# Kernel tuning notes

Hardware: AMD Instinct MI355X
Metric: run time of the kernel (lower is better)

The kernel has to match this reference:

```python
import math
import jax, jax.numpy as jnp
import numpy as np

B, T, C, FD, K, V = 8, 2048, 256, 256, 128, 256

def setup_inputs() -> dict:
    key = jax.random.key(0)
    ks = jax.random.split(key, 8)
    s = 0.02
    return {
        "inp": jax.random.normal(ks[0], (B, T, C), jnp.float32),
        "feature": jax.random.normal(ks[1], (B, T, FD), jnp.float32),
        "Wq": jax.random.normal(ks[2], (C + FD, K), jnp.float32) * s,
        "bq": jnp.zeros((K,), jnp.float32),
        "Wk": jax.random.normal(ks[3], (C, K), jnp.float32) * s,
        "bk": jnp.zeros((K,), jnp.float32),
        "Wv": jax.random.normal(ks[4], (C, V), jnp.float32) * s,
        "bv": jnp.zeros((V,), jnp.float32),
    }

def reference(inp, feature, Wq, bq, Wk, bk, Wv, bv):
    # inp: [B,T,C], feature: [B,T,FD]
    t = inp.shape[1]
    q = jnp.concatenate([inp, feature], axis=-1) @ Wq + bq   # [B,T,K]
    k = inp @ Wk + bk                                        # [B,T,K]
    v = inp @ Wv + bv                                        # [B,T,V]
    # scores[b, j, i] = q_j . k_i ; original masks where i > j (strict upper tri)
    scores = jnp.einsum('bjk,bik->bji', q, k)                # [B,T,T]
    mask = jnp.triu(jnp.ones((t, t), dtype=bool), k=1)       # mask[j,i] = i > j
    scores = jnp.where(mask[None], -jnp.inf, scores) / math.sqrt(K)
    # NOTE: original softmax is over dim=1 (the query/row axis), not the key axis
    attn = jax.nn.softmax(scores, axis=1)                    # [B,T,T]
    out = jnp.einsum('bji,biv->bjv', attn, v)                # [B,T,V]
    return jnp.concatenate([inp, out], axis=-1)              # [B,T,C+V]
```

## Files before the change

### kernel.cpp

```cpp
#include <hip/hip_runtime.h>
#include <hip/hip_bf16.h>
#include <cstdint>

#define Bb  8
#define Tt  2048
#define Cc  256
#define FDd 256
#define Kk  128
#define Vv  256
#define BT  (Bb * Tt)
#define NTRI 136

#define INV_SQRT_K 0.08838834764831845f

typedef __bf16 bf16x8 __attribute__((ext_vector_type(8)));
typedef __bf16 bf16x4 __attribute__((ext_vector_type(4)));
typedef float  f32x4  __attribute__((ext_vector_type(4)));

__device__ __forceinline__ void gload16(const void* g, void* l) {
  __builtin_amdgcn_global_load_lds(
      (const __attribute__((address_space(1))) void*)g,
      (__attribute__((address_space(3))) void*)l, 16, 0, 0);
}

__global__ __launch_bounds__(256) void prepw_kernel(
    const float4* __restrict__ inp4, const float4* __restrict__ feat4,
    float4* __restrict__ out4, bf16x4* __restrict__ inpB4,
    bf16x4* __restrict__ featB4,
    const float* __restrict__ Wq, const float* __restrict__ Wk,
    const float* __restrict__ Wv, __bf16* __restrict__ Wqt,
    __bf16* __restrict__ Wkt, __bf16* __restrict__ Wvt)
{
  if (blockIdx.x < 4096) {
    const int g = blockIdx.x * 256 + threadIdx.x;
    const int row = g >> 6, c = g & 63;
    const float4 x = inp4[g];
    out4[(size_t)row * 128 + c] = x;
    bf16x4 xb; xb[0] = (__bf16)x.x; xb[1] = (__bf16)x.y; xb[2] = (__bf16)x.z; xb[3] = (__bf16)x.w;
    inpB4[g] = xb;
    const float4 f = feat4[g];
    bf16x4 fb; fb[0] = (__bf16)f.x; fb[1] = (__bf16)f.y; fb[2] = (__bf16)f.z; fb[3] = (__bf16)f.w;
    featB4[g] = fb;
  } else {
    const int g = (blockIdx.x - 4096) * 256 + threadIdx.x;
    if (g < 65536) {
      const int n = g >> 9, k = g & 511;
      Wqt[g] = (__bf16)Wq[k * 128 + n];
    } else if (g < 98304) {
      const int h = g - 65536;
      const int n = h >> 8, k = h & 255;
      Wkt[h] = (__bf16)Wk[k * 128 + n];
    } else {
      const int h = g - 98304;
      const int n = h >> 8, k = h & 255;
      Wvt[h] = (__bf16)Wv[k * 256 + n];
    }
  }
}

__global__ __launch_bounds__(256, 3) void qkv_mfma_kernel(
    const __bf16* __restrict__ inpB, const __bf16* __restrict__ featB,
    const __bf16* __restrict__ Wqt, const __bf16* __restrict__ Wkt,
    const __bf16* __restrict__ Wvt,
    const float* __restrict__ bq, const float* __restrict__ bk,
    const float* __restrict__ bv,
    __bf16* __restrict__ qb, __bf16* __restrict__ kb, __bf16* __restrict__ vT)
{
  __shared__ __bf16 Atile[128 * 64];
  __shared__ __bf16 Btile[128 * 64];
  const int panel = blockIdx.y;
  const int m0 = blockIdx.x * 128;
  const int lane = threadIdx.x & 63, wave = threadIdx.x >> 6;
  const int cl = lane & 15, quad = lane >> 4;
  const int jl0 = (wave >> 1) * 64;
  const int vl0 = (wave & 1) * 64;

  const __bf16* Wt; const float* bias; int kblocks;
  if (panel == 0)      { Wt = Wqt; bias = bq; kblocks = 8; }
  else if (panel == 1) { Wt = Wkt; bias = bk; kblocks = 4; }
  else                 { Wt = Wvt + (size_t)(panel - 2) * 128 * 256;
                         bias = bv + (panel - 2) * 128; kblocks = 4; }
  const int Kd = kblocks * 64;

  const int lrow = lane >> 3;
  const int lchunk = ((lane & 7) ^ lrow) * 8;

  f32x4 acc[4][4];
#pragma unroll
  for (int mt = 0; mt < 4; ++mt)
#pragma unroll
    for (int nt = 0; nt < 4; ++nt) acc[mt][nt] = (f32x4){0.f, 0.f, 0.f, 0.f};

  for (int kb = 0; kb < kblocks; ++kb) {
    const __bf16* Asrc = (panel == 0 && kb >= 4) ? featB : inpB;
    const int koff = (panel == 0 && kb >= 4) ? (kb - 4) * 64 : kb * 64;
    __syncthreads();
#pragma unroll
    for (int t = 0; t < 4; ++t) {
      const int r0 = wave * 32 + t * 8;
      gload16(Asrc + (size_t)(m0 + r0 + lrow) * 256 + koff + lchunk, Atile + r0 * 64);
      gload16(Wt + (size_t)(r0 + lrow) * Kd + kb * 64 + lchunk, Btile + r0 * 64);
    }
    __syncthreads();
#pragma unroll
    for (int ks = 0; ks < 2; ++ks) {
      bf16x8 af[4], bfr[4];
#pragma unroll
      for (int mt = 0; mt < 4; ++mt) {
        const int jlr = jl0 + mt * 16 + cl;
        af[mt] = *(const bf16x8*)(Atile + jlr * 64 + (((ks * 4 + quad) ^ (jlr & 7)) * 8));
      }
#pragma unroll
      for (int nt = 0; nt < 4; ++nt) {
        const int vlr = vl0 + nt * 16 + cl;
        bfr[nt] = *(const bf16x8*)(Btile + vlr * 64 + (((ks * 4 + quad) ^ (vlr & 7)) * 8));
      }
#pragma unroll
      for (int mt = 0; mt < 4; ++mt)
#pragma unroll
        for (int nt = 0; nt < 4; ++nt)
          acc[mt][nt] = __builtin_amdgcn_mfma_f32_16x16x32_bf16(af[mt], bfr[nt], acc[mt][nt], 0, 0, 0);
    }
  }

  if (panel < 2) {
    __bf16* dst = (panel == 0) ? qb : kb;
    const float scale = (panel == 0) ? INV_SQRT_K : 1.0f;
#pragma unroll
    for (int mt = 0; mt < 4; ++mt) {
      const int row = m0 + jl0 + mt * 16 + quad * 4;
#pragma unroll
      for (int nt = 0; nt < 4; ++nt) {
        const int col = vl0 + nt * 16 + cl;
        const float bs = bias[col];
#pragma unroll
        for (int r = 0; r < 4; ++r)
          dst[(size_t)(row + r) * Kk + col] = (__bf16)((acc[mt][nt][r] + bs) * scale);
      }
    }
  } else {
    const int b = m0 >> 11;
#pragma unroll
    for (int mt = 0; mt < 4; ++mt) {
      const int t0 = (m0 & (Tt - 1)) + jl0 + mt * 16 + quad * 4;
#pragma unroll
      for (int nt = 0; nt < 4; ++nt) {
        const int vcol = (panel - 2) * 128 + vl0 + nt * 16 + cl;
        const float bs = bias[vl0 + nt * 16 + cl];
        bf16x4 v4;
#pragma unroll
        for (int r = 0; r < 4; ++r) v4[r] = (__bf16)(acc[mt][nt][r] + bs);
        *(bf16x4*)(vT + (size_t)(b * Vv + vcol) * Tt + t0) = v4;
      }
    }
  }
}

__global__ __launch_bounds__(256, 2) void sexp_kernel(
    const __bf16* __restrict__ qb, const __bf16* __restrict__ kb,
    __bf16* __restrict__ expS, float* __restrict__ partialD)
{
  __shared__ __bf16 tiles[2 * 128 * 128];
  __shared__ float lcs[4][64];
  __bf16* Qtile = tiles;
  __bf16* Ktile = tiles + 128 * 128;
  float*  P     = (float*)tiles;

  const int b = blockIdx.x, l = blockIdx.y;
  int jt = 0, base = 0;
  while (base + jt + 1 <= l) { base += jt + 1; ++jt; }
  const int it = l - base;

  const int lane = threadIdx.x & 63, wave = threadIdx.x >> 6;
  const int cl = lane & 15, quad = lane >> 4;
  const int jl0 = (wave >> 1) * 64;
  const int il0 = (wave & 1) * 64;
  const size_t rowbase = (size_t)b * Tt;

  {
    const int srow = lane >> 4;
    const int cslot = lane & 15;
    const __bf16* qsrc = qb + (rowbase + jt * 128) * Kk;
    const __bf16* ksrc = kb + (rowbase + it * 128) * Kk;
#pragma unroll
    for (int t = 0; t < 8; ++t) {
      const int r0 = wave * 32 + t * 4;
      const int row = r0 + srow;
      const int cg = (cslot ^ (row & 7)) * 8;
      gload16(qsrc + (size_t)row * Kk + cg, Qtile + r0 * 128);
      gload16(ksrc + (size_t)row * Kk + cg, Ktile + r0 * 128);
    }
  }
  __syncthreads();

  f32x4 acc[4][4];
#pragma unroll
  for (int mt = 0; mt < 4; ++mt)
#pragma unroll
    for (int nt = 0; nt < 4; ++nt) acc[mt][nt] = (f32x4){0.f, 0.f, 0.f, 0.f};

#pragma unroll
  for (int s = 0; s < 4; ++s) {
    bf16x8 af[4], bfr[4];
#pragma unroll
    for (int mt = 0; mt < 4; ++mt) {
      const int jlr = jl0 + mt * 16 + cl;
      af[mt] = *(const bf16x8*)(Qtile + jlr * 128 + (((s * 4 + quad) ^ (jlr & 7)) * 8));
    }
#pragma unroll
    for (int nt = 0; nt < 4; ++nt) {
      const int ilr = il0 + nt * 16 + cl;
      bfr[nt] = *(const bf16x8*)(Ktile + ilr * 128 + (((s * 4 + quad) ^ (ilr & 7)) * 8));
    }
#pragma unroll
    for (int mt = 0; mt < 4; ++mt)
#pragma unroll
      for (int nt = 0; nt < 4; ++nt)
        acc[mt][nt] = __builtin_amdgcn_mfma_f32_16x16x32_bf16(af[mt], bfr[nt], acc[mt][nt], 0, 0, 0);
  }
  __syncthreads();

  const bool diag = (it == jt);
  float cs[4] = {0.f, 0.f, 0.f, 0.f};
#pragma unroll
  for (int mt = 0; mt < 4; ++mt) {
    const int jl = jl0 + mt * 16 + quad * 4;
#pragma unroll
    for (int nt = 0; nt < 4; ++nt) {
      const int il = il0 + nt * 16 + cl;
#pragma unroll
      for (int r = 0; r < 4; ++r) {
        float p = __expf(acc[mt][nt][r]);
        if (diag && il > (jl + r)) p = 0.f;
        cs[nt] += (float)(__bf16)p;
        P[(jl + r) * 128 + il] = p;
      }
    }
  }
#pragma unroll
  for (int nt = 0; nt < 4; ++nt) {
    cs[nt] += __shfl_xor(cs[nt], 16);
    cs[nt] += __shfl_xor(cs[nt], 32);
  }
  if (quad == 0) {
#pragma unroll
    for (int nt = 0; nt < 4; ++nt) lcs[wave][nt * 16 + cl] = cs[nt];
  }
  __syncthreads();

  __bf16* slot = expS + ((size_t)(b * NTRI + l)) * (128 * 128);
  {
    const int srow = lane >> 4;
    const int c0 = (lane & 15) * 8;
#pragma unroll
    for (int t = 0; t < 8; ++t) {
      const int row = wave * 32 + t * 4 + srow;
      const f32x4 p0 = *(const f32x4*)(P + row * 128 + c0);
      const f32x4 p1 = *(const f32x4*)(P + row * 128 + c0 + 4);
      bf16x8 pb;
#pragma unroll
      for (int u = 0; u < 4; ++u) { pb[u] = (__bf16)p0[u]; pb[4 + u] = (__bf16)p1[u]; }
      *(bf16x8*)(slot + (size_t)row * 128 + c0) = pb;
    }
  }

  const int tid = threadIdx.x;
  if (tid < 128) {
    const int w0 = (tid < 64) ? 0 : 1;
    const int lc = tid & 63;
    const float s = lcs[w0][lc] + lcs[w0 + 2][lc];
    partialD[((size_t)b * 16 + jt) * Tt + it * 128 + tid] = s;
  }
}

__global__ __launch_bounds__(256) void dvscale_kernel(
    const float* __restrict__ partialD, bf16x8* __restrict__ vT8)
{
  __shared__ float rec[32];
  const int b = blockIdx.x, ic = blockIdx.y;
  const int i0 = ic * 32;
  const int tid = threadIdx.x;
  if (tid < 32) {
    const int i = i0 + tid;
    float s = 0.f;
#pragma unroll
    for (int jt = 0; jt < 16; ++jt) s += partialD[((size_t)b * 16 + jt) * Tt + i];
    rec[tid] = 1.0f / s;
  }
  __syncthreads();
  const int iu = tid & 3, v0 = tid >> 2;
#pragma unroll
  for (int p = 0; p < 4; ++p) {
    const int v = v0 + p * 64;
    const size_t idx = ((size_t)b * Vv + v) * (Tt / 8) + (i0 >> 3) + iu;
    bf16x8 x = vT8[idx];
    const int rb = iu * 8;
#pragma unroll
    for (int t = 0; t < 8; ++t) x[t] = (__bf16)((float)x[t] * rec[rb + t]);
    vT8[idx] = x;
  }
}

__global__ __launch_bounds__(256, 4) void pvgemm_kernel(
    const __bf16* __restrict__ expS, const __bf16* __restrict__ vT,
    float* __restrict__ out)
{
  __shared__ __bf16 At[2][128 * 64];
  __shared__ __bf16 Bt[2][64 * 64];
  const int b = blockIdx.x;
  const int p = blockIdx.y >> 2;
  const int nq = blockIdx.y & 3;
  const int lane = threadIdx.x & 63, wave = threadIdx.x >> 6;
  const int cl = lane & 15, quad = lane >> 4;
  const int jl0 = (wave >> 1) * 64;
  const int vl0 = (wave & 1) * 32;
  const int lrow = lane >> 3;
  const int lchunk = ((lane & 7) ^ lrow) * 8;
  const __bf16* vbase = vT + ((size_t)b * Vv + nq * 64) * Tt;

#pragma unroll
  for (int sp = 0; sp < 2; ++sp) {
    const int jt = sp ? p : 15 - p;
    const int kblocks = (jt + 1) * 2;
    const size_t slotbase = (size_t)(b * NTRI + (jt * (jt + 1)) / 2) * 16384;

    f32x4 acc[4][2];
#pragma unroll
    for (int mt = 0; mt < 4; ++mt)
#pragma unroll
      for (int nt = 0; nt < 2; ++nt) acc[mt][nt] = (f32x4){0.f, 0.f, 0.f, 0.f};

    {
      const __bf16* Ag = expS + slotbase;
#pragma unroll
      for (int t = 0; t < 4; ++t) {
        const int r0 = wave * 32 + t * 8;
        gload16(Ag + (size_t)(r0 + lrow) * 128 + lchunk, At[0] + r0 * 64);
      }
#pragma unroll
      for (int t = 0; t < 2; ++t) {
        const int r0 = wave * 16 + t * 8;
        gload16(vbase + (size_t)(r0 + lrow) * Tt + lchunk, Bt[0] + r0 * 64);
      }
    }
    __syncthreads();

    int buf = 0;
    for (int kb = 0; kb < kblocks; ++kb) {
      if (kb + 1 < kblocks) {
        const int kn = kb + 1;
        const __bf16* Ag = expS + slotbase + (size_t)(kn >> 1) * 16384 + (kn & 1) * 64;
        const int i0 = kn * 64;
#pragma unroll
        for (int t = 0; t < 4; ++t) {
          const int r0 = wave * 32 + t * 8;
          gload16(Ag + (size_t)(r0 + lrow) * 128 + lchunk, At[buf ^ 1] + r0 * 64);
        }
#pragma unroll
        for (int t = 0; t < 2; ++t) {
          const int r0 = wave * 16 + t * 8;
          gload16(vbase + (size_t)(r0 + lrow) * Tt + i0 + lchunk, Bt[buf ^ 1] + r0 * 64);
        }
      }
#pragma unroll
      for (int ks = 0; ks < 2; ++ks) {
        bf16x8 af[4], bfr[2];
#pragma unroll
        for (int mt = 0; mt < 4; ++mt) {
          const int jlr = jl0 + mt * 16 + cl;
          af[mt] = *(const bf16x8*)(At[buf] + jlr * 64 + (((ks * 4 + quad) ^ (jlr & 7)) * 8));
        }
#pragma unroll
        for (int nt = 0; nt < 2; ++nt) {
          const int vlr = vl0 + nt * 16 + cl;
          bfr[nt] = *(const bf16x8*)(Bt[buf] + vlr * 64 + (((ks * 4 + quad) ^ (vlr & 7)) * 8));
        }
#pragma unroll
        for (int mt = 0; mt < 4; ++mt)
#pragma unroll
          for (int nt = 0; nt < 2; ++nt)
            acc[mt][nt] = __builtin_amdgcn_mfma_f32_16x16x32_bf16(af[mt], bfr[nt], acc[mt][nt], 0, 0, 0);
      }
      __syncthreads();
      buf ^= 1;
    }

    float* orow = out + ((size_t)b * Tt + jt * 128 + jl0) * (size_t)(Cc + Vv)
                + Cc + nq * 64 + vl0;
#pragma unroll
    for (int mt = 0; mt < 4; ++mt)
#pragma unroll
      for (int nt = 0; nt < 2; ++nt)
#pragma unroll
        for (int r = 0; r < 4; ++r)
          orow[(size_t)(mt * 16 + quad * 4 + r) * (Cc + Vv) + nt * 16 + cl] = acc[mt][nt][r];
  }
}

extern "C" void kernel_launch(void* const* d_in, const int* in_sizes, int n_in,
                              void* d_out, int out_size, void* d_ws, size_t ws_size,
                              hipStream_t stream) {
  const float* inp  = (const float*)d_in[0];
  const float* feat = (const float*)d_in[1];
  const float* Wq   = (const float*)d_in[2];
  const float* bq   = (const float*)d_in[3];
  const float* Wk   = (const float*)d_in[4];
  const float* bk   = (const float*)d_in[5];
  const float* Wv   = (const float*)d_in[6];
  const float* bv   = (const float*)d_in[7];
  float* out = (float*)d_out;

  char* ws = (char*)d_ws;
  __bf16* inpB   = (__bf16*)(ws);
  __bf16* featB  = (__bf16*)(ws + (8u << 20));
  __bf16* qb     = (__bf16*)(ws + (16u << 20));
  __bf16* kb     = (__bf16*)(ws + (20u << 20));
  __bf16* vT     = (__bf16*)(ws + (24u << 20));
  __bf16* Wqt    = (__bf16*)(ws + (32u << 20));
  __bf16* Wkt    = (__bf16*)(ws + (32u << 20) + (128u << 10));
  __bf16* Wvt    = (__bf16*)(ws + (32u << 20) + (192u << 10));
  float*  partialD = (float*)(ws + (33u << 20));
  __bf16* expS     = (__bf16*)(ws + (36u << 20));

  prepw_kernel<<<dim3(4096 + 640), 256, 0, stream>>>(
      (const float4*)inp, (const float4*)feat, (float4*)out,
      (bf16x4*)inpB, (bf16x4*)featB, Wq, Wk, Wv, Wqt, Wkt, Wvt);
  qkv_mfma_kernel<<<dim3(BT / 128, 4), 256, 0, stream>>>(
      inpB, featB, Wqt, Wkt, Wvt, bq, bk, bv, qb, kb, vT);
  sexp_kernel<<<dim3(Bb, NTRI), 256, 0, stream>>>(qb, kb, expS, partialD);
  dvscale_kernel<<<dim3(Bb, 64), 256, 0, stream>>>(partialD, (bf16x8*)vT);
  pvgemm_kernel<<<dim3(Bb, 32), 256, 0, stream>>>(expS, vT, out);
}
```

Measured before the change: 160.1 us.

## Fold softmax reciprocal scaling into PV GEMM and swizzle P staging buffer

Replaces the separate kernel that rescaled the whole bf16 V^T tensor in place with a small reduction kernel that only writes per-key reciprocals; the PV GEMM now multiplies its B fragments by those reciprocals after loading them from LDS. This removes a read-modify-write pass over V but adds float conversions and multiplies, plus global reciprocal loads, inside the GEMM inner loop. It also XOR-swizzles the column index of the fp32 P staging tile in the score kernel to cut LDS bank conflicts between the scattered MFMA-layout writes and the row-vector reads.

```diff
diff --git a/kernel.cpp b/kernel.cpp
--- a/kernel.cpp
+++ b/kernel.cpp
@@ -233,7 +233,8 @@
         float p = __expf(acc[mt][nt][r]);
         if (diag && il > (jl + r)) p = 0.f;
         cs[nt] += (float)(__bf16)p;
-        P[(jl + r) * 128 + il] = p;
+        const int row = jl + r;
+        P[row * 128 + (il ^ (((row >> 2) & 1) << 4))] = p;
       }
     }
   }
@@ -255,8 +256,9 @@
 #pragma unroll
     for (int t = 0; t < 8; ++t) {
       const int row = wave * 32 + t * 4 + srow;
-      const f32x4 p0 = *(const f32x4*)(P + row * 128 + c0);
-      const f32x4 p1 = *(const f32x4*)(P + row * 128 + c0 + 4);
+      const int c0p = c0 ^ (((row >> 2) & 1) << 4);
+      const f32x4 p0 = *(const f32x4*)(P + row * 128 + c0p);
+      const f32x4 p1 = *(const f32x4*)(P + row * 128 + c0p + 4);
       bf16x8 pb;
 #pragma unroll
       for (int u = 0; u < 4; ++u) { pb[u] = (__bf16)p0[u]; pb[4 + u] = (__bf16)p1[u]; }
@@ -273,37 +275,20 @@
   }
 }
 
-__global__ __launch_bounds__(256) void dvscale_kernel(
-    const float* __restrict__ partialD, bf16x8* __restrict__ vT8)
+__global__ __launch_bounds__(256) void dreduce_kernel(
+    const float* __restrict__ partialD, float* __restrict__ recipD)
 {
-  __shared__ float rec[32];
-  const int b = blockIdx.x, ic = blockIdx.y;
-  const int i0 = ic * 32;
-  const int tid = threadIdx.x;
-  if (tid < 32) {
-    const int i = i0 + tid;
-    float s = 0.f;
-#pragma unroll
-    for (int jt = 0; jt < 16; ++jt) s += partialD[((size_t)b * 16 + jt) * Tt + i];
-    rec[tid] = 1.0f / s;
-  }
-  __syncthreads();
-  const int iu = tid & 3, v0 = tid >> 2;
-#pragma unroll
-  for (int p = 0; p < 4; ++p) {
-    const int v = v0 + p * 64;
-    const size_t idx = ((size_t)b * Vv + v) * (Tt / 8) + (i0 >> 3) + iu;
-    bf16x8 x = vT8[idx];
-    const int rb = iu * 8;
-#pragma unroll
-    for (int t = 0; t < 8; ++t) x[t] = (__bf16)((float)x[t] * rec[rb + t]);
-    vT8[idx] = x;
-  }
+  const int g = blockIdx.x * 256 + threadIdx.x;
+  const int b = g >> 11, i = g & (Tt - 1);
+  float s = 0.f;
+#pragma unroll
+  for (int jt = 0; jt < 16; ++jt) s += partialD[((size_t)b * 16 + jt) * Tt + i];
+  recipD[g] = 1.0f / s;
 }
 
 __global__ __launch_bounds__(256, 4) void pvgemm_kernel(
     const __bf16* __restrict__ expS, const __bf16* __restrict__ vT,
-    float* __restrict__ out)
+    const float* __restrict__ recipD, float* __restrict__ out)
 {
   __shared__ __bf16 At[2][128 * 64];
   __shared__ __bf16 Bt[2][64 * 64];
@@ -317,6 +302,7 @@
   const int lrow = lane >> 3;
   const int lchunk = ((lane & 7) ^ lrow) * 8;
   const __bf16* vbase = vT + ((size_t)b * Vv + nq * 64) * Tt;
+  const float* rbase = recipD + (size_t)b * Tt;
 
 #pragma unroll
   for (int sp = 0; sp < 2; ++sp) {
@@ -350,7 +336,7 @@
       if (kb + 1 < kblocks) {
         const int kn = kb + 1;
         const __bf16* Ag = expS + slotbase + (size_t)(kn >> 1) * 16384 + (kn & 1) * 64;
-        const int i0 = kn * 64;
+        const int i0n = kn * 64;
 #pragma unroll
         for (int t = 0; t < 4; ++t) {
           const int r0 = wave * 32 + t * 8;
@@ -359,11 +345,14 @@
 #pragma unroll
         for (int t = 0; t < 2; ++t) {
           const int r0 = wave * 16 + t * 8;
-          gload16(vbase + (size_t)(r0 + lrow) * Tt + i0 + lchunk, Bt[buf ^ 1] + r0 * 64);
+          gload16(vbase + (size_t)(r0 + lrow) * Tt + i0n + lchunk, Bt[buf ^ 1] + r0 * 64);
         }
       }
+      const float* rstep = rbase + kb * 64;
 #pragma unroll
       for (int ks = 0; ks < 2; ++ks) {
+        const f32x4 ra = *(const f32x4*)(rstep + (ks * 4 + quad) * 8);
+        const f32x4 rb = *(const f32x4*)(rstep + (ks * 4 + quad) * 8 + 4);
         bf16x8 af[4], bfr[2];
 #pragma unroll
         for (int mt = 0; mt < 4; ++mt) {
@@ -374,6 +363,11 @@
         for (int nt = 0; nt < 2; ++nt) {
           const int vlr = vl0 + nt * 16 + cl;
           bfr[nt] = *(const bf16x8*)(Bt[buf] + vlr * 64 + (((ks * 4 + quad) ^ (vlr & 7)) * 8));
+#pragma unroll
+          for (int u = 0; u < 4; ++u) {
+            bfr[nt][u]     = (__bf16)((float)bfr[nt][u]     * ra[u]);
+            bfr[nt][4 + u] = (__bf16)((float)bfr[nt][4 + u] * rb[u]);
+          }
         }
 #pragma unroll
         for (int mt = 0; mt < 4; ++mt)
@@ -420,6 +414,7 @@
   __bf16* Wkt    = (__bf16*)(ws + (32u << 20) + (128u << 10));
   __bf16* Wvt    = (__bf16*)(ws + (32u << 20) + (192u << 10));
   float*  partialD = (float*)(ws + (33u << 20));
+  float*  recipD   = (float*)(ws + (35u << 20));
   __bf16* expS     = (__bf16*)(ws + (36u << 20));
 
   prepw_kernel<<<dim3(4096 + 640), 256, 0, stream>>>(
@@ -428,6 +423,6 @@
   qkv_mfma_kernel<<<dim3(BT / 128, 4), 256, 0, stream>>>(
       inpB, featB, Wqt, Wkt, Wvt, bq, bk, bv, qb, kb, vT);
   sexp_kernel<<<dim3(Bb, NTRI), 256, 0, stream>>>(qb, kb, expS, partialD);
-  dvscale_kernel<<<dim3(Bb, 64), 256, 0, stream>>>(partialD, (bf16x8*)vT);
-  pvgemm_kernel<<<dim3(Bb, 32), 256, 0, stream>>>(expS, vT, out);
-}
+  dreduce_kernel<<<dim3(BT / 256), 256, 0, stream>>>(partialD, recipD);
+  pvgemm_kernel<<<dim3(Bb, 32), 256, 0, stream>>>(expS, vT, recipD, out);
+}
```

Measured after the change: 168.1 us. 1.05x slower.

## Split-K the PV GEMM with atomic accumulation and swizzle P staging in LDS

Applied to the files above, without the earlier changes.

The PV GEMM grid is changed from paired row tiles to per-tile chunks of up to eight k-blocks, giving many more blocks with even work. Partial results are combined with relaxed atomic float adds, so the output's V half is zero-initialised in the prep kernel. Separately, the fp32 P staging buffer in the score kernel is XOR-swizzled to reduce LDS bank conflicts. Atomics add traffic and make the summation order nondeterministic.

```diff
diff --git a/kernel.cpp b/kernel.cpp
--- a/kernel.cpp
+++ b/kernel.cpp
@@ -36,6 +36,7 @@
     const int row = g >> 6, c = g & 63;
     const float4 x = inp4[g];
     out4[(size_t)row * 128 + c] = x;
+    out4[(size_t)row * 128 + 64 + c] = (float4){0.f, 0.f, 0.f, 0.f};
     bf16x4 xb; xb[0] = (__bf16)x.x; xb[1] = (__bf16)x.y; xb[2] = (__bf16)x.z; xb[3] = (__bf16)x.w;
     inpB4[g] = xb;
     const float4 f = feat4[g];
@@ -233,7 +234,8 @@
         float p = __expf(acc[mt][nt][r]);
         if (diag && il > (jl + r)) p = 0.f;
         cs[nt] += (float)(__bf16)p;
-        P[(jl + r) * 128 + il] = p;
+        const int row = jl + r;
+        P[row * 128 + (il ^ (((row >> 2) & 1) << 4))] = p;
       }
     }
   }
@@ -255,8 +257,9 @@
 #pragma unroll
     for (int t = 0; t < 8; ++t) {
       const int row = wave * 32 + t * 4 + srow;
-      const f32x4 p0 = *(const f32x4*)(P + row * 128 + c0);
-      const f32x4 p1 = *(const f32x4*)(P + row * 128 + c0 + 4);
+      const int c0p = c0 ^ (((row >> 2) & 1) << 4);
+      const f32x4 p0 = *(const f32x4*)(P + row * 128 + c0p);
+      const f32x4 p1 = *(const f32x4*)(P + row * 128 + c0p + 4);
       bf16x8 pb;
 #pragma unroll
       for (int u = 0; u < 4; ++u) { pb[u] = (__bf16)p0[u]; pb[4 + u] = (__bf16)p1[u]; }
@@ -301,15 +304,21 @@
   }
 }
 
-__global__ __launch_bounds__(256, 4) void pvgemm_kernel(
+__global__ __launch_bounds__(256, 3) void pvgemm_kernel(
     const __bf16* __restrict__ expS, const __bf16* __restrict__ vT,
     float* __restrict__ out)
 {
   __shared__ __bf16 At[2][128 * 64];
   __shared__ __bf16 Bt[2][64 * 64];
   const int b = blockIdx.x;
-  const int p = blockIdx.y >> 2;
   const int nq = blockIdx.y & 3;
+  const int z = blockIdx.y >> 2;
+  int jt = 0, zb = 0;
+  while (zb + (jt >> 2) + 1 <= z) { zb += (jt >> 2) + 1; ++jt; }
+  const int c = z - zb;
+  const int kb0 = c * 8;
+  const int kend = min(kb0 + 8, (jt + 1) * 2);
+
   const int lane = threadIdx.x & 63, wave = threadIdx.x >> 6;
   const int cl = lane & 15, quad = lane >> 4;
   const int jl0 = (wave >> 1) * 64;
@@ -317,84 +326,82 @@
   const int lrow = lane >> 3;
   const int lchunk = ((lane & 7) ^ lrow) * 8;
   const __bf16* vbase = vT + ((size_t)b * Vv + nq * 64) * Tt;
-
-#pragma unroll
-  for (int sp = 0; sp < 2; ++sp) {
-    const int jt = sp ? p : 15 - p;
-    const int kblocks = (jt + 1) * 2;
-    const size_t slotbase = (size_t)(b * NTRI + (jt * (jt + 1)) / 2) * 16384;
-
-    f32x4 acc[4][2];
-#pragma unroll
-    for (int mt = 0; mt < 4; ++mt)
-#pragma unroll
-      for (int nt = 0; nt < 2; ++nt) acc[mt][nt] = (f32x4){0.f, 0.f, 0.f, 0.f};
-
-    {
-      const __bf16* Ag = expS + slotbase;
+  const size_t slotbase = (size_t)(b * NTRI + (jt * (jt + 1)) / 2) * 16384;
+
+  f32x4 acc[4][2];
+#pragma unroll
+  for (int mt = 0; mt < 4; ++mt)
+#pragma unroll
+    for (int nt = 0; nt < 2; ++nt) acc[mt][nt] = (f32x4){0.f, 0.f, 0.f, 0.f};
+
+  {
+    const __bf16* Ag = expS + slotbase + (size_t)(kb0 >> 1) * 16384 + (kb0 & 1) * 64;
+    const int i0 = kb0 * 64;
+#pragma unroll
+    for (int t = 0; t < 4; ++t) {
+      const int r0 = wave * 32 + t * 8;
+      gload16(Ag + (size_t)(r0 + lrow) * 128 + lchunk, At[0] + r0 * 64);
+    }
+#pragma unroll
+    for (int t = 0; t < 2; ++t) {
+      const int r0 = wave * 16 + t * 8;
+      gload16(vbase + (size_t)(r0 + lrow) * Tt + i0 + lchunk, Bt[0] + r0 * 64);
+    }
+  }
+  __syncthreads();
+
+  int buf = 0;
+  for (int kb = kb0; kb < kend; ++kb) {
+    if (kb + 1 < kend) {
+      const int kn = kb + 1;
+      const __bf16* Ag = expS + slotbase + (size_t)(kn >> 1) * 16384 + (kn & 1) * 64;
+      const int i0n = kn * 64;
 #pragma unroll
       for (int t = 0; t < 4; ++t) {
         const int r0 = wave * 32 + t * 8;
-        gload16(Ag + (size_t)(r0 + lrow) * 128 + lchunk, At[0] + r0 * 64);
+        gload16(Ag + (size_t)(r0 + lrow) * 128 + lchunk, At[buf ^ 1] + r0 * 64);
       }
 #pragma unroll
       for (int t = 0; t < 2; ++t) {
         const int r0 = wave * 16 + t * 8;
-        gload16(vbase + (size_t)(r0 + lrow) * Tt + lchunk, Bt[0] + r0 * 64);
-      }
+        gload16(vbase + (size_t)(r0 + lrow) * Tt + i0n + lchunk, Bt[buf ^ 1] + r0 * 64);
+      }
+    }
+#pragma unroll
+    for (int ks = 0; ks < 2; ++ks) {
+      bf16x8 af[4], bfr[2];
+#pragma unroll
+      for (int mt = 0; mt < 4; ++mt) {
+        const int jlr = jl0 + mt * 16 + cl;
+        af[mt] = *(const bf16x8*)(At[buf] + jlr * 64 + (((ks * 4 + quad) ^ (jlr & 7)) * 8));
+      }
+#pragma unroll
+      for (int nt = 0; nt < 2; ++nt) {
+        const int vlr = vl0 + nt * 16 + cl;
+        bfr[nt] = *(const bf16x8*)(Bt[buf] + vlr * 64 + (((ks * 4 + quad) ^ (vlr & 7)) * 8));
+      }
+#pragma unroll
+      for (int mt = 0; mt < 4; ++mt)
+#pragma unroll
+        for (int nt = 0; nt < 2; ++nt)
+          acc[mt][nt] = __builtin_amdgcn_mfma_f32_16x16x32_bf16(af[mt], bfr[nt], acc[mt][nt], 0, 0, 0);
     }
     __syncthreads();
-
-    int buf = 0;
-    for (int kb = 0; kb < kblocks; ++kb) {
-      if (kb + 1 < kblocks) {
-        const int kn = kb + 1;
-        const __bf16* Ag = expS + slotbase + (size_t)(kn >> 1) * 16384 + (kn & 1) * 64;
-        const int i0 = kn * 64;
-#pragma unroll
-        for (int t = 0; t < 4; ++t) {
-          const int r0 = wave * 32 + t * 8;
-          gload16(Ag + (size_t)(r0 + lrow) * 128 + lchunk, At[buf ^ 1] + r0 * 64);
-        }
-#pragma unroll
-        for (int t = 0; t < 2; ++t) {
-          const int r0 = wave * 16 + t * 8;
-          gload16(vbase + (size_t)(r0 + lrow) * Tt + i0 + lchunk, Bt[buf ^ 1] + r0 * 64);
-        }
-      }
-#pragma unroll
-      for (int ks = 0; ks < 2; ++ks) {
-        bf16x8 af[4], bfr[2];
-#pragma unroll
-        for (int mt = 0; mt < 4; ++mt) {
-          const int jlr = jl0 + mt * 16 + cl;
-          af[mt] = *(const bf16x8*)(At[buf] + jlr * 64 + (((ks * 4 + quad) ^ (jlr & 7)) * 8));
-        }
-#pragma unroll
-        for (int nt = 0; nt < 2; ++nt) {
-          const int vlr = vl0 + nt * 16 + cl;
-          bfr[nt] = *(const bf16x8*)(Bt[buf] + vlr * 64 + (((ks * 4 + quad) ^ (vlr & 7)) * 8));
-        }
-#pragma unroll
-        for (int mt = 0; mt < 4; ++mt)
-#pragma unroll
-          for (int nt = 0; nt < 2; ++nt)
-            acc[mt][nt] = __builtin_amdgcn_mfma_f32_16x16x32_bf16(af[mt], bfr[nt], acc[mt][nt], 0, 0, 0);
-      }
-      __syncthreads();
-      buf ^= 1;
-    }
-
-    float* orow = out + ((size_t)b * Tt + jt * 128 + jl0) * (size_t)(Cc + Vv)
-                + Cc + nq * 64 + vl0;
-#pragma unroll
-    for (int mt = 0; mt < 4; ++mt)
-#pragma unroll
-      for (int nt = 0; nt < 2; ++nt)
-#pragma unroll
-        for (int r = 0; r < 4; ++r)
-          orow[(size_t)(mt * 16 + quad * 4 + r) * (Cc + Vv) + nt * 16 + cl] = acc[mt][nt][r];
-  }
+    buf ^= 1;
+  }
+
+  float* orow = out + ((size_t)b * Tt + jt * 128 + jl0) * (size_t)(Cc + Vv)
+              + Cc + nq * 64 + vl0;
+#pragma unroll
+  for (int mt = 0; mt < 4; ++mt)
+#pragma unroll
+    for (int nt = 0; nt < 2; ++nt)
+#pragma unroll
+      for (int r = 0; r < 4; ++r) {
+        float* addr = orow + (size_t)(mt * 16 + quad * 4 + r) * (Cc + Vv) + nt * 16 + cl;
+        __hip_atomic_fetch_add(addr, acc[mt][nt][r], __ATOMIC_RELAXED,
+                               __HIP_MEMORY_SCOPE_AGENT);
+      }
 }
 
 extern "C" void kernel_launch(void* const* d_in, const int* in_sizes, int n_in,
@@ -429,5 +436,5 @@
       inpB, featB, Wqt, Wkt, Wvt, bq, bk, bv, qb, kb, vT);
   sexp_kernel<<<dim3(Bb, NTRI), 256, 0, stream>>>(qb, kb, expS, partialD);
   dvscale_kernel<<<dim3(Bb, 64), 256, 0, stream>>>(partialD, (bf16x8*)vT);
-  pvgemm_kernel<<<dim3(Bb, 32), 256, 0, stream>>>(expS, vT, out);
-}
+  pvgemm_kernel<<<dim3(Bb, 160), 256, 0, stream>>>(expS, vT, out);
+}
```

Result: slower. 170.3 us (+6.4%).

## Split PV GEMM into 64-row tiles and swizzle sexp LDS staging

Applied to the files above, without the earlier changes.

The PV GEMM kernel now works on 64-row output tiles instead of 128-row ones. It pairs tile p with tile 31-p so each block does the same total amount of work, and it launches twice as many blocks, with smaller LDS A buffers and fewer accumulators per wave. The aim is better occupancy and load balance on the triangular workload. The sexp kernel also XOR-swizzles the float scratch tile P to reduce LDS bank conflicts on the write and readback. A trailing barrier is added between the two sub-problems, and each expS A tile is now loaded once per 64-row half, so the same bytes may be fetched more often.

```diff
diff --git a/kernel.cpp b/kernel.cpp
--- a/kernel.cpp
+++ b/kernel.cpp
@@ -233,7 +233,8 @@
         float p = __expf(acc[mt][nt][r]);
         if (diag && il > (jl + r)) p = 0.f;
         cs[nt] += (float)(__bf16)p;
-        P[(jl + r) * 128 + il] = p;
+        const int row = jl + r;
+        P[row * 128 + (il ^ (((row >> 2) & 1) << 4))] = p;
       }
     }
   }
@@ -255,8 +256,9 @@
 #pragma unroll
     for (int t = 0; t < 8; ++t) {
       const int row = wave * 32 + t * 4 + srow;
-      const f32x4 p0 = *(const f32x4*)(P + row * 128 + c0);
-      const f32x4 p1 = *(const f32x4*)(P + row * 128 + c0 + 4);
+      const int c0p = c0 ^ (((row >> 2) & 1) << 4);
+      const f32x4 p0 = *(const f32x4*)(P + row * 128 + c0p);
+      const f32x4 p1 = *(const f32x4*)(P + row * 128 + c0p + 4);
       bf16x8 pb;
 #pragma unroll
       for (int u = 0; u < 4; ++u) { pb[u] = (__bf16)p0[u]; pb[4 + u] = (__bf16)p1[u]; }
@@ -305,14 +307,14 @@
     const __bf16* __restrict__ expS, const __bf16* __restrict__ vT,
     float* __restrict__ out)
 {
-  __shared__ __bf16 At[2][128 * 64];
+  __shared__ __bf16 At[2][64 * 64];
   __shared__ __bf16 Bt[2][64 * 64];
   const int b = blockIdx.x;
   const int p = blockIdx.y >> 2;
   const int nq = blockIdx.y & 3;
   const int lane = threadIdx.x & 63, wave = threadIdx.x >> 6;
   const int cl = lane & 15, quad = lane >> 4;
-  const int jl0 = (wave >> 1) * 64;
+  const int jl0 = (wave >> 1) * 32;
   const int vl0 = (wave & 1) * 32;
   const int lrow = lane >> 3;
   const int lchunk = ((lane & 7) ^ lrow) * 8;
@@ -320,53 +322,46 @@
 
 #pragma unroll
   for (int sp = 0; sp < 2; ++sp) {
-    const int jt = sp ? p : 15 - p;
-    const int kblocks = (jt + 1) * 2;
-    const size_t slotbase = (size_t)(b * NTRI + (jt * (jt + 1)) / 2) * 16384;
-
-    f32x4 acc[4][2];
-#pragma unroll
-    for (int mt = 0; mt < 4; ++mt)
+    const int jt64 = sp ? p : 31 - p;
+    const int jt128 = jt64 >> 1;
+    const int rowoff = (jt64 & 1) * 64;
+    const int ksteps = jt64 + 1;
+    const size_t tribase = (size_t)(b * NTRI + (jt128 * (jt128 + 1)) / 2) * 16384;
+
+    f32x4 acc[2][2];
+#pragma unroll
+    for (int mt = 0; mt < 2; ++mt)
 #pragma unroll
       for (int nt = 0; nt < 2; ++nt) acc[mt][nt] = (f32x4){0.f, 0.f, 0.f, 0.f};
 
-    {
-      const __bf16* Ag = expS + slotbase;
-#pragma unroll
-      for (int t = 0; t < 4; ++t) {
-        const int r0 = wave * 32 + t * 8;
-        gload16(Ag + (size_t)(r0 + lrow) * 128 + lchunk, At[0] + r0 * 64);
-      }
-#pragma unroll
-      for (int t = 0; t < 2; ++t) {
-        const int r0 = wave * 16 + t * 8;
-        gload16(vbase + (size_t)(r0 + lrow) * Tt + lchunk, Bt[0] + r0 * 64);
-      }
+#pragma unroll
+    for (int t = 0; t < 2; ++t) {
+      const int r0 = wave * 16 + t * 8;
+      gload16(expS + tribase + (size_t)(rowoff + r0 + lrow) * 128 + lchunk,
+              At[0] + r0 * 64);
+      gload16(vbase + (size_t)(r0 + lrow) * Tt + lchunk, Bt[0] + r0 * 64);
     }
     __syncthreads();
 
     int buf = 0;
-    for (int kb = 0; kb < kblocks; ++kb) {
-      if (kb + 1 < kblocks) {
+    for (int kb = 0; kb < ksteps; ++kb) {
+      if (kb + 1 < ksteps) {
         const int kn = kb + 1;
-        const __bf16* Ag = expS + slotbase + (size_t)(kn >> 1) * 16384 + (kn & 1) * 64;
-        const int i0 = kn * 64;
-#pragma unroll
-        for (int t = 0; t < 4; ++t) {
-          const int r0 = wave * 32 + t * 8;
-          gload16(Ag + (size_t)(r0 + lrow) * 128 + lchunk, At[buf ^ 1] + r0 * 64);
-        }
+        const __bf16* Ag = expS + tribase + (size_t)(kn >> 1) * 16384
+                         + (size_t)rowoff * 128 + (kn & 1) * 64;
+        const int i0n = kn * 64;
 #pragma unroll
         for (int t = 0; t < 2; ++t) {
           const int r0 = wave * 16 + t * 8;
-          gload16(vbase + (size_t)(r0 + lrow) * Tt + i0 + lchunk, Bt[buf ^ 1] + r0 * 64);
+          gload16(Ag + (size_t)(r0 + lrow) * 128 + lchunk, At[buf ^ 1] + r0 * 64);
+          gload16(vbase + (size_t)(r0 + lrow) * Tt + i0n + lchunk, Bt[buf ^ 1] + r0 * 64);
         }
       }
 #pragma unroll
       for (int ks = 0; ks < 2; ++ks) {
-        bf16x8 af[4], bfr[2];
-#pragma unroll
-        for (int mt = 0; mt < 4; ++mt) {
+        bf16x8 af[2], bfr[2];
+#pragma unroll
+        for (int mt = 0; mt < 2; ++mt) {
           const int jlr = jl0 + mt * 16 + cl;
           af[mt] = *(const bf16x8*)(At[buf] + jlr * 64 + (((ks * 4 + quad) ^ (jlr & 7)) * 8));
         }
@@ -376,7 +371,7 @@
           bfr[nt] = *(const bf16x8*)(Bt[buf] + vlr * 64 + (((ks * 4 + quad) ^ (vlr & 7)) * 8));
         }
 #pragma unroll
-        for (int mt = 0; mt < 4; ++mt)
+        for (int mt = 0; mt < 2; ++mt)
 #pragma unroll
           for (int nt = 0; nt < 2; ++nt)
             acc[mt][nt] = __builtin_amdgcn_mfma_f32_16x16x32_bf16(af[mt], bfr[nt], acc[mt][nt], 0, 0, 0);
@@ -385,15 +380,17 @@
       buf ^= 1;
     }
 
-    float* orow = out + ((size_t)b * Tt + jt * 128 + jl0) * (size_t)(Cc + Vv)
+    float* orow = out + ((size_t)b * Tt + jt64 * 64 + jl0) * (size_t)(Cc + Vv)
                 + Cc + nq * 64 + vl0;
 #pragma unroll
-    for (int mt = 0; mt < 4; ++mt)
+    for (int mt = 0; mt < 2; ++mt)
 #pragma unroll
       for (int nt = 0; nt < 2; ++nt)
 #pragma unroll
         for (int r = 0; r < 4; ++r)
           orow[(size_t)(mt * 16 + quad * 4 + r) * (Cc + Vv) + nt * 16 + cl] = acc[mt][nt][r];
+
+    __syncthreads();
   }
 }
 
@@ -429,5 +426,5 @@
       inpB, featB, Wqt, Wkt, Wvt, bq, bk, bv, qb, kb, vT);
   sexp_kernel<<<dim3(Bb, NTRI), 256, 0, stream>>>(qb, kb, expS, partialD);
   dvscale_kernel<<<dim3(Bb, 64), 256, 0, stream>>>(partialD, (bf16x8*)vT);
-  pvgemm_kernel<<<dim3(Bb, 32), 256, 0, stream>>>(expS, vT, out);
-}
+  pvgemm_kernel<<<dim3(Bb, 64), 256, 0, stream>>>(expS, vT, out);
+}
```

Measured after the change: 157.0 us. No clear change (-1.9%).
